# Optimization experiments

Hardware: AMD Instinct MI355X
Metric: run time of the kernel (lower is better)

The kernel has to match this reference:

```python
import jax, jax.numpy as jnp
import numpy as np

B, N, D_MAX_LEN, D_LENGTH, D_MODEL, N_CLASS = 16, 1024, 512, 256, 128, 10
SAMPLE_K = 140  # factor(20) * ceil(ln(1024)) = 20*7; also n_top u (L_Q == L_K)


def setup_inputs() -> dict:
    key = jax.random.key(0)
    ks = jax.random.split(key, 10)
    s = 0.02
    return {
        "input_embedding": jax.random.normal(ks[0], (B, N, D_MAX_LEN), jnp.float32),
        "index_sample": jax.random.randint(ks[1], (N, SAMPLE_K), 0, N),
        # weights stored [in, out] (transpose of torch Linear.weight)
        "W_lin": jax.random.normal(ks[2], (D_MAX_LEN, D_LENGTH), jnp.float32) * s,
        "b_lin": jnp.zeros((D_LENGTH,), jnp.float32),
        "W_q": jax.random.normal(ks[3], (D_LENGTH, D_MODEL), jnp.float32) * s,
        "W_k": jax.random.normal(ks[4], (D_LENGTH, D_MODEL), jnp.float32) * s,
        "W_v": jax.random.normal(ks[5], (D_LENGTH, D_MODEL), jnp.float32) * s,
        "W_add": jax.random.normal(ks[6], (D_LENGTH, D_MODEL), jnp.float32) * s,
        "b_add": jnp.zeros((D_MODEL,), jnp.float32),
        "W_final": jax.random.normal(ks[7], (D_MODEL * N, N_CLASS), jnp.float32) * s,
        "b_final": jnp.zeros((N_CLASS,), jnp.float32),
    }


def reference(input_embedding, index_sample, W_lin, b_lin, W_q, W_k, W_v,
              W_add, b_add, W_final, b_final):
    # self.linear: [B, N, d_max_len] -> [B, N, d_length]
    x = input_embedding @ W_lin + b_lin
    b, n, _ = x.shape
    # single head (h=1): [B, 1, L, D]
    Q = (x @ W_q)[:, None]
    K = (x @ W_k)[:, None]
    V = (x @ W_v)[:, None]
    d = Q.shape[-1]
    L_K = n
    n_top = index_sample.shape[1]  # u == sample_k here

    # _prob_QK: gather sampled keys per query row, score against Q
    Kg = K[:, :, index_sample, :]                      # [B,1,L_Q,S,D]
    QK_sample = jnp.einsum('bhld,bhlsd->bhls', Q, Kg)  # [B,1,L_Q,S]
    M = QK_sample.max(-1) - QK_sample.sum(-1) / L_K    # sparsity measure
    _, M_top = jax.lax.top_k(M, n_top)                 # [B,1,u]

    Qr = jnp.take_along_axis(Q, M_top[..., None], axis=2)       # [B,1,u,D]
    scores = jnp.einsum('bhud,bhkd->bhuk', Qr, K) / np.sqrt(d)  # [B,1,u,L_K]

    # _get_initial_context (mask_flag=False): mean of V broadcast over L_Q
    ctx = jnp.broadcast_to(V.mean(axis=2, keepdims=True), V.shape)  # [B,1,L_Q,D]

    # _update_context: scatter softmax(scores) @ V into selected rows
    attn = jax.nn.softmax(scores, axis=-1)
    upd = jnp.einsum('bhuk,bhkd->bhud', attn, V)  # [B,1,u,D]
    bidx = jnp.arange(b)[:, None, None]
    hidx = jnp.arange(1)[None, :, None]
    ctx = ctx.at[bidx, hidx, M_top].set(upd)

    ctx = ctx[:, 0]                    # H=1 -> [B,N,D]
    out = ctx + (x @ W_add + b_add)    # residual add (dropout: eval mode)
    out = out.reshape(b, -1) @ W_final + b_final  # [B, n_class]
    return out
```

## Files before the change

kernel.cpp:

```cpp
#include <hip/hip_runtime.h>

typedef __attribute__((ext_vector_type(8))) short short8;
typedef __attribute__((ext_vector_type(8))) unsigned short ushort8;
typedef __attribute__((ext_vector_type(4))) float f32x4;
typedef unsigned short u16;
typedef unsigned int u32;
typedef __attribute__((address_space(1))) const u32 gu32;
typedef __attribute__((address_space(3))) u32 lu32;

__device__ __forceinline__ u16 f2bf(float f){
  unsigned u = __float_as_uint(f);
  u += 0x7FFF + ((u >> 16) & 1);
  return (u16)(u >> 16);
}
__device__ __forceinline__ float bf2f(u16 h){ return __uint_as_float(((unsigned)h) << 16); }

#define BB   16
#define NN   1024
#define DML  512
#define DL   256
#define DM   128
#define NC   10
#define SK   140
#define KTOT (NN*DM)

__global__ void k_prep(const float* __restrict__ Wlin, const float* __restrict__ Wq,
                       const float* __restrict__ Wk, const float* __restrict__ Wv,
                       const float* __restrict__ Wadd,
                       u16* __restrict__ wlinT, u16* __restrict__ w4T,
                       const float* __restrict__ Wf, u16* __restrict__ wf2,
                       const int* __restrict__ idxs, u16* __restrict__ idxp){
  int blk = blockIdx.x, t = threadIdx.x;
  if (blk < 512){
    int id = blk*256 + t;
    {
      int j = id >> 9;
      int k = id & 511;
      wlinT[id] = f2bf(Wlin[k*DL + j]);
    }
    {
      int j = id >> 8;
      int k = id & 255;
      const float* src = (j < 128) ? Wq : (j < 256) ? Wk : (j < 384) ? Wv : Wadd;
      int jj = j & 127;
      w4T[id] = f2bf(src[k*DM + jj]);
    }
  } else if (blk < 1792){
    int i4 = (blk-512)*256 + t;
    float4 v = ((const float4*)Wf)[i4];
    ushort4 o; o.x=f2bf(v.x); o.y=f2bf(v.y); o.z=f2bf(v.z); o.w=f2bf(v.w);
    ((ushort4*)wf2)[i4] = o;
  } else {
    int id = (blk-1792)*256 + t;
    int l = id / 144;
    int s = id - l*144;
    idxp[id] = (s < SK) ? (u16)idxs[l*SK + s] : (u16)0xFFFF;
  }
}

__device__ __forceinline__ void stage2(const u16* __restrict__ A, const u16* __restrict__ B,
                                       int K, int m0, int n0, int kb,
                                       u16* sA, u16* sB, int tid, int wave){
  #pragma unroll
  for (int i = 0; i < 4; ++i){
    int ci  = i*256 + tid;
    int row = ci >> 3;
    int kc  = (ci & 7) ^ (row & 7);
    __builtin_amdgcn_global_load_lds((gu32*)(A + (long)(m0+row)*K + kb + kc*8),
                                     (lu32*)(sA + (i*256 + wave*64)*8), 16, 0, 0);
    __builtin_amdgcn_global_load_lds((gu32*)(B + (long)(n0+row)*K + kb + kc*8),
                                     (lu32*)(sB + (i*256 + wave*64)*8), 16, 0, 0);
  }
}
__device__ __forceinline__ void compute64(const u16* sA, const u16* sB,
                                          int lane, int wrow, int wcol, f32x4 acc[4][4]){
  #pragma unroll
  for (int kk = 0; kk < 2; ++kk){
    short8 af[4], bfr[4];
    int cb = kk*4 + (lane >> 4);
    #pragma unroll
    for (int m_=0; m_<4; ++m_){
      int row = wrow + m_*16 + (lane & 15);
      af[m_] = *(const short8*)&sA[row*64 + ((cb ^ (row & 7)) << 3)];
    }
    #pragma unroll
    for (int n_=0; n_<4; ++n_){
      int row = wcol + n_*16 + (lane & 15);
      bfr[n_] = *(const short8*)&sB[row*64 + ((cb ^ (row & 7)) << 3)];
    }
    #pragma unroll
    for (int m_=0; m_<4; ++m_)
      #pragma unroll
      for (int n_=0; n_<4; ++n_)
        acc[m_][n_] = __builtin_amdgcn_mfma_f32_16x16x32_bf16(af[m_], bfr[n_], acc[m_][n_], 0, 0, 0);
  }
}
__device__ __forceinline__ void gemm_core_db(const u16* __restrict__ A, const u16* __restrict__ B,
                                             int K, int m0, int n0,
                                             u16* sA0, u16* sB0, u16* sA1, u16* sB1,
                                             f32x4 acc[4][4]){
  const int tid  = threadIdx.x;
  const int lane = tid & 63;
  const int wave = tid >> 6;
  const int wrow = (wave >> 1) * 64;
  const int wcol = (wave & 1) * 64;
  u16 *cA = sA0, *cB = sB0, *nA = sA1, *nB = sB1;
  stage2(A, B, K, m0, n0, 0, cA, cB, tid, wave);
  __syncthreads();
  int nt = K >> 6;
  for (int t = 0; t < nt-1; ++t){
    stage2(A, B, K, m0, n0, (t+1)*64, nA, nB, tid, wave);
    compute64(cA, cB, lane, wrow, wcol, acc);
    __syncthreads();
    u16* x;
    x = cA; cA = nA; nA = x;
    x = cB; cB = nB; nB = x;
  }
  compute64(cA, cB, lane, wrow, wcol, acc);
}

__global__ __launch_bounds__(256) void k_gemm_x(const float* __restrict__ A, const u16* __restrict__ B,
                                                const float* __restrict__ bias, u16* __restrict__ out){
  __shared__ u16 smem[12288];
  u16* sA = smem;
  u16* sB = smem + 4096;
  const int tid  = threadIdx.x;
  const int lane = tid & 63;
  const int wave = tid >> 6;
  const int wrow = (wave >> 1) * 32;
  const int wcol = (wave & 1) * 64;
  int m0 = blockIdx.x*64, n0 = blockIdx.y*128;
  f32x4 acc[2][4];
  f32x4 z = {0.f,0.f,0.f,0.f};
  #pragma unroll
  for (int m_=0;m_<2;++m_) for (int n_=0;n_<4;++n_) acc[m_][n_] = z;

  f32x4 ra[4];
  short8 rb[4];
  const int arow = tid >> 2, aq = tid & 3;

  {
    const float* src = A + (long)(m0+arow)*DML + aq*16;
    ra[0] = ((const f32x4*)src)[0]; ra[1] = ((const f32x4*)src)[1];
    ra[2] = ((const f32x4*)src)[2]; ra[3] = ((const f32x4*)src)[3];
    #pragma unroll
    for (int i=0;i<4;++i){
      int ci = i*256 + tid, row = ci>>3, kc = ci&7;
      rb[i] = *(const short8*)(B + (long)(n0+row)*DML + kc*8);
    }
  }
  {
    short8 o0, o1;
    #pragma unroll
    for (int j=0;j<4;++j){ o0[j]=(short)f2bf(ra[0][j]); o0[4+j]=(short)f2bf(ra[1][j]);
                           o1[j]=(short)f2bf(ra[2][j]); o1[4+j]=(short)f2bf(ra[3][j]); }
    int kc0 = aq*2, kc1 = aq*2+1;
    *(short8*)&sA[arow*64 + ((kc0 ^ (arow&7))<<3)] = o0;
    *(short8*)&sA[arow*64 + ((kc1 ^ (arow&7))<<3)] = o1;
    #pragma unroll
    for (int i=0;i<4;++i){
      int ci = i*256 + tid, row = ci>>3, kc = ci&7;
      *(short8*)&sB[row*64 + ((kc ^ (row&7))<<3)] = rb[i];
    }
  }
  __syncthreads();

  for (int tt = 0; tt < 8; ++tt){
    if (tt < 7){
      int kb = (tt+1)*64;
      const float* src = A + (long)(m0+arow)*DML + kb + aq*16;
      ra[0] = ((const f32x4*)src)[0]; ra[1] = ((const f32x4*)src)[1];
      ra[2] = ((const f32x4*)src)[2]; ra[3] = ((const f32x4*)src)[3];
      #pragma unroll
      for (int i=0;i<4;++i){
        int ci = i*256 + tid, row = ci>>3, kc = ci&7;
        rb[i] = *(const short8*)(B + (long)(n0+row)*DML + kb + kc*8);
      }
    }
    #pragma unroll
    for (int kk = 0; kk < 2; ++kk){
      short8 af[2], bfr[4];
      int cb = kk*4 + (lane >> 4);
      #pragma unroll
      for (int m_=0; m_<2; ++m_){
        int row = wrow + m_*16 + (lane & 15);
        af[m_] = *(const short8*)&sA[row*64 + ((cb ^ (row & 7)) << 3)];
      }
      #pragma unroll
      for (int n_=0; n_<4; ++n_){
        int row = wcol + n_*16 + (lane & 15);
        bfr[n_] = *(const short8*)&sB[row*64 + ((cb ^ (row & 7)) << 3)];
      }
      #pragma unroll
      for (int m_=0; m_<2; ++m_)
        #pragma unroll
        for (int n_=0; n_<4; ++n_)
          acc[m_][n_] = __builtin_amdgcn_mfma_f32_16x16x32_bf16(af[m_], bfr[n_], acc[m_][n_], 0, 0, 0);
    }
    __syncthreads();
    if (tt < 7){
      short8 o0, o1;
      #pragma unroll
      for (int j=0;j<4;++j){ o0[j]=(short)f2bf(ra[0][j]); o0[4+j]=(short)f2bf(ra[1][j]);
                             o1[j]=(short)f2bf(ra[2][j]); o1[4+j]=(short)f2bf(ra[3][j]); }
      int kc0 = aq*2, kc1 = aq*2+1;
      *(short8*)&sA[arow*64 + ((kc0 ^ (arow&7))<<3)] = o0;
      *(short8*)&sA[arow*64 + ((kc1 ^ (arow&7))<<3)] = o1;
      #pragma unroll
      for (int i=0;i<4;++i){
        int ci = i*256 + tid, row = ci>>3, kc = ci&7;
        *(short8*)&sB[row*64 + ((kc ^ (row&7))<<3)] = rb[i];
      }
      __syncthreads();
    }
  }

  u16* sC = sB;
  #pragma unroll
  for (int m_=0;m_<2;++m_)
    #pragma unroll
    for (int n_=0;n_<4;++n_)
      #pragma unroll
      for (int rr=0;rr<4;++rr){
        int row = wrow + m_*16 + (lane>>4)*4 + rr;
        int col = wcol + n_*16 + (lane & 15);
        sC[row*128 + col] = f2bf(acc[m_][n_][rr] + bias[n0 + col]);
      }
  __syncthreads();
  #pragma unroll
  for (int i = 0; i < 4; ++i){
    int ci = i*256 + tid;
    int row = ci >> 4, c = ci & 15;
    *(short8*)(out + (long)(m0+row)*DL + n0 + c*8) = *(const short8*)&sC[row*128 + c*8];
  }
}

__global__ __launch_bounds__(256) void k_gemm_qkva(const u16* __restrict__ A, const u16* __restrict__ B,
                                                   const float* __restrict__ badd,
                                                   u16* __restrict__ oq, u16* __restrict__ ok,
                                                   u16* __restrict__ ov, u16* __restrict__ oa){
  __shared__ u16 smem[32768];
  f32x4 acc[4][4];
  f32x4 z = {0.f,0.f,0.f,0.f};
  #pragma unroll
  for (int m_=0;m_<4;++m_) for (int n_=0;n_<4;++n_) acc[m_][n_] = z;
  int m0 = blockIdx.x*128;
  int tn = blockIdx.y;
  gemm_core_db(A, B, DL, m0, tn*128, smem, smem+8192, smem+16384, smem+24576, acc);
  int tid = threadIdx.x, lane = tid & 63, wave = tid >> 6;
  int wrow = (wave>>1)*64, wcol = (wave&1)*64;
  u16* dst = (tn==0) ? oq : (tn==1) ? ok : (tn==2) ? ov : oa;

  u16* sC = smem;
  #pragma unroll
  for (int m_=0;m_<4;++m_)
    #pragma unroll
    for (int n_=0;n_<4;++n_)
      #pragma unroll
      for (int r=0;r<4;++r){
        int row = wrow + m_*16 + (lane>>4)*4 + r;
        int col = wcol + n_*16 + (lane & 15);
        float v = acc[m_][n_][r];
        if (tn == 3) v += badd[col];
        sC[row*128 + col] = f2bf(v);
      }
  __syncthreads();
  u16* db = dst + (long)m0*DM;
  #pragma unroll
  for (int i = 0; i < 8; ++i){
    int ci = i*256 + tid;
    int row = ci >> 4, c = ci & 15;
    *(short8*)(db + (long)row*DM + c*8) = *(const short8*)&sC[row*128 + c*8];
  }
}

__global__ __launch_bounds__(256) void k_gemm_s(const u16* __restrict__ Q, const u16* __restrict__ Km,
                                                u16* __restrict__ S, const u16* __restrict__ idxp,
                                                float* __restrict__ pmax, float* __restrict__ psum){
  __shared__ u16 smem[16384];
  u16* sA = smem;
  u16* sB = smem + 8192;
  const int tid = threadIdx.x, lane = tid & 63, wave = tid >> 6;
  const int wrow = (wave>>1)*64, wcol = (wave&1)*64;
  f32x4 acc[4][4];
  f32x4 z = {0.f,0.f,0.f,0.f};
  #pragma unroll
  for (int m_=0;m_<4;++m_) for (int n_=0;n_<4;++n_) acc[m_][n_] = z;
  int b = blockIdx.x, n0 = blockIdx.y*128, m0 = blockIdx.z*128;
  const u16* A = Q  + (long)b*NN*DM;
  const u16* B = Km + (long)b*NN*DM;

  stage2(A, B, DM, m0, n0, 0, sA, sB, tid, wave);
  __syncthreads();
  compute64(sA, sB, lane, wrow, wcol, acc);
  __syncthreads();
  stage2(A, B, DM, m0, n0, 64, sA, sB, tid, wave);
  __syncthreads();
  compute64(sA, sB, lane, wrow, wcol, acc);
  __syncthreads();

  u16* sS = smem;
  #pragma unroll
  for (int m_=0;m_<4;++m_)
    #pragma unroll
    for (int n_=0;n_<4;++n_)
      #pragma unroll
      for (int r=0;r<4;++r){
        int row = wrow + m_*16 + (lane>>4)*4 + r;
        int col = wcol + n_*16 + (lane & 15);
        sS[row*128 + col] = f2bf(acc[m_][n_][r]);
      }
  __syncthreads();

  u16* Sb = S + (long)b*NN*NN + (long)m0*NN + n0;
  #pragma unroll
  for (int i = 0; i < 8; ++i){
    int ci = i*256 + tid;
    int row = ci >> 4, c = ci & 15;
    *(short8*)(Sb + (long)row*NN + c*8) = *(const short8*)&sS[row*128 + c*8];
  }

  int l = tid >> 1, h = tid & 1;
  const u16* ip = idxp + (long)(m0+l)*144 + h*72;
  float mx = -1e30f, sm = 0.f;
  #pragma unroll
  for (int j = 0; j < 9; ++j){
    ushort8 v = *(const ushort8*)(ip + j*8);
    #pragma unroll
    for (int e = 0; e < 8; ++e){
      int d = (int)v[e] - n0;
      if ((unsigned)d < 128u){
        float s = bf2f(sS[l*128 + d]);
        mx = fmaxf(mx, s); sm += s;
      }
    }
  }
  float mo = __shfl_xor(mx, 1), so = __shfl_xor(sm, 1);
  mx = fmaxf(mx, mo); sm += so;
  if (h == 0){
    int o = (b*8 + blockIdx.y)*NN + m0 + l;
    pmax[o] = mx; psum[o] = sm;
  }
}

__global__ __launch_bounds__(256) void k_rankvm(const float* __restrict__ pmax, const float* __restrict__ psum,
                                                int* __restrict__ partial,
                                                const u16* __restrict__ V, float* __restrict__ vmean){
  int blk = blockIdx.x, t = threadIdx.x;
  if (blk < 256){
    __shared__ float Ml[1024];
    int b = blk >> 4, jc = blk & 15;
    #pragma unroll
    for (int r=0;r<4;++r){
      int i = t + r*256;
      float mx = -1e30f, sm = 0.f;
      #pragma unroll
      for (int nb=0;nb<8;++nb){
        mx = fmaxf(mx, pmax[(b*8+nb)*NN + i]);
        sm += psum[(b*8+nb)*NN + i];
      }
      Ml[i] = mx - sm * (1.0f/1024.0f);
    }
    __syncthreads();
    float mi[4];
    int cnt[4] = {0,0,0,0};
    #pragma unroll
    for (int r=0;r<4;++r) mi[r] = Ml[t + r*256];
    int j0 = jc*64;
    for (int j = 0; j < 64; ++j){
      float mj = Ml[j0 + j];
      int jg = j0 + j;
      #pragma unroll
      for (int r=0;r<4;++r){
        int i = t + r*256;
        cnt[r] += (mj > mi[r]) || (mj == mi[r] && jg < i);
      }
    }
    int* pb = partial + (b*16 + jc)*NN;
    #pragma unroll
    for (int r=0;r<4;++r) pb[t + r*256] = cnt[r];
  } else {
    __shared__ float red[16][128];
    int b = blk - 256;
    int d8 = t & 15, seg = t >> 4;
    const u16* Vb = V + (long)b*KTOT + seg*64*DM + d8*8;
    float acc[8] = {0,0,0,0,0,0,0,0};
    for (int l = 0; l < 64; ++l){
      short8 v = *(const short8*)(Vb + l*DM);
      #pragma unroll
      for (int j=0;j<8;++j) acc[j] += bf2f((u16)v[j]);
    }
    #pragma unroll
    for (int j=0;j<8;++j) red[seg][d8*8+j] = acc[j];
    __syncthreads();
    if (t < 128){
      float s = 0.f;
      #pragma unroll
      for (int g=0;g<16;++g) s += red[g][t];
      vmean[b*DM + t] = s * (1.0f/1024.0f);
    }
  }
}

__global__ __launch_bounds__(1024) void k_sel(const int* __restrict__ partial, int* __restrict__ mtop,
                                              int* __restrict__ selmap){
  int b = blockIdx.x, i = threadIdx.x;
  int cnt = 0;
  #pragma unroll
  for (int jc = 0; jc < 16; ++jc) cnt += partial[(b*16 + jc)*NN + i];
  selmap[b*NN + i] = (cnt < SK) ? cnt : -1;
  if (cnt < SK) mtop[b*SK + cnt] = i;
}

__global__ __launch_bounds__(256) void k_attn(const u16* __restrict__ S, const u16* __restrict__ V,
                                              const int* __restrict__ mtop, float* __restrict__ upd){
  __shared__ float sE[4][1024];
  __shared__ float redM[4][4];
  __shared__ float redS[4][4];
  __shared__ float sP[4][4][128];
  int b = blockIdx.x, u0 = blockIdx.y*4, t = threadIdx.x;
  int lane = t & 63, wave = t >> 6;
  const float inv = 0.08838834764831845f;

  int rows[4];
  #pragma unroll
  for (int r=0;r<4;++r) rows[r] = mtop[b*SK + u0 + r];

  float sv[4][4];
  float pm[4];
  const u16* Sb = S + (long)b*NN*NN;
  #pragma unroll
  for (int r=0;r<4;++r){
    ushort4 raw = ((const ushort4*)(Sb + (long)rows[r]*NN))[t];
    sv[r][0] = bf2f(raw.x)*inv; sv[r][1] = bf2f(raw.y)*inv;
    sv[r][2] = bf2f(raw.z)*inv; sv[r][3] = bf2f(raw.w)*inv;
    pm[r] = fmaxf(fmaxf(sv[r][0],sv[r][1]), fmaxf(sv[r][2],sv[r][3]));
  }
  #pragma unroll
  for (int o=32;o;o>>=1)
    #pragma unroll
    for (int r=0;r<4;++r) pm[r] = fmaxf(pm[r], __shfl_xor(pm[r],o));
  if (lane == 0){
    #pragma unroll
    for (int r=0;r<4;++r) redM[wave][r] = pm[r];
  }
  __syncthreads();
  float mx[4], ps[4];
  #pragma unroll
  for (int r=0;r<4;++r)
    mx[r] = fmaxf(fmaxf(redM[0][r],redM[1][r]), fmaxf(redM[2][r],redM[3][r]));
  #pragma unroll
  for (int r=0;r<4;++r){
    float s = 0.f;
    #pragma unroll
    for (int j=0;j<4;++j){
      float e = __expf(sv[r][j] - mx[r]);
      sE[r][t*4+j] = e;
      s += e;
    }
    ps[r] = s;
  }
  #pragma unroll
  for (int o=32;o;o>>=1)
    #pragma unroll
    for (int r=0;r<4;++r) ps[r] += __shfl_xor(ps[r],o);
  if (lane == 0){
    #pragma unroll
    for (int r=0;r<4;++r) redS[wave][r] = ps[r];
  }
  __syncthreads();
  float rZ[4];
  #pragma unroll
  for (int r=0;r<4;++r)
    rZ[r] = 1.0f / (redS[0][r]+redS[1][r]+redS[2][r]+redS[3][r]);

  int dg = t & 15;
  int kg = t >> 4;
  const u16* Vb = V + (long)b*KTOT + dg*8;
  float acc[4][8];
  #pragma unroll
  for (int r=0;r<4;++r)
    #pragma unroll
    for (int j=0;j<8;++j) acc[r][j] = 0.f;

  for (int k = kg; k < NN; k += 16){
    short8 v = *(const short8*)(Vb + (long)k*DM);
    float vf[8];
    #pragma unroll
    for (int j=0;j<8;++j) vf[j] = bf2f((u16)v[j]);
    #pragma unroll
    for (int r=0;r<4;++r){
      float e = sE[r][k];
      #pragma unroll
      for (int j=0;j<8;++j) acc[r][j] += e * vf[j];
    }
  }

  #pragma unroll
  for (int o=16;o<64;o<<=1)
    #pragma unroll
    for (int r=0;r<4;++r)
      #pragma unroll
      for (int j=0;j<8;++j) acc[r][j] += __shfl_xor(acc[r][j], o);

  if ((t & 63) < 16){
    #pragma unroll
    for (int r=0;r<4;++r)
      #pragma unroll
      for (int j=0;j<8;++j) sP[wave][r][dg*8+j] = acc[r][j];
  }
  __syncthreads();
  if (t < 128){
    #pragma unroll
    for (int r=0;r<4;++r){
      float s = sP[0][r][t] + sP[1][r][t] + sP[2][r][t] + sP[3][r][t];
      upd[((long)b*SK + u0 + r)*DM + t] = s * rZ[r];
    }
  }
}

__global__ __launch_bounds__(256) void k_final(const float* __restrict__ upd, const float* __restrict__ vmean,
                                               const int* __restrict__ selmap,
                                               const u16* __restrict__ Aad,
                                               const u16* __restrict__ wf2, float* __restrict__ part){
  int b = blockIdx.x, ch = blockIdx.y, t = threadIdx.x;
  long base = (long)b * KTOT;
  int k0 = ch * 4096;
  float acc[NC] = {0.f};
  for (int k = k0 + t; k < k0 + 4096; k += 256){
    int l = k >> 7, d = k & 127;
    int sel = selmap[b*NN + l];
    float c = (sel >= 0) ? upd[((long)b*SK + sel)*DM + d] : vmean[b*DM + d];
    float v = c + bf2f(Aad[base + k]);
    const u32* w32 = (const u32*)(wf2 + (long)k*NC);
    #pragma unroll
    for (int cc = 0; cc < 5; ++cc){
      u32 w = w32[cc];
      acc[2*cc]   += v * bf2f((u16)(w & 0xFFFF));
      acc[2*cc+1] += v * bf2f((u16)(w >> 16));
    }
  }
  __shared__ float lred[40];
  int lane = t & 63, wave = t >> 6;
  #pragma unroll
  for (int c = 0; c < NC; ++c){
    float v = acc[c];
    #pragma unroll
    for (int o=32;o;o>>=1) v += __shfl_xor(v,o);
    if (lane == 0) lred[wave*NC + c] = v;
  }
  __syncthreads();
  if (t < NC) part[(b*32 + ch)*NC + t] = lred[t] + lred[NC+t] + lred[2*NC+t] + lred[3*NC+t];
}

__global__ void k_out(const float* __restrict__ part, const float* __restrict__ bfin, float* __restrict__ out){
  int t = threadIdx.x;
  if (t < BB*NC){
    int b = t / NC, c = t % NC;
    float s = bfin[c];
    #pragma unroll
    for (int ch = 0; ch < 32; ++ch) s += part[(b*32 + ch)*NC + c];
    out[t] = s;
  }
}

extern "C" void kernel_launch(void* const* d_in, const int* in_sizes, int n_in,
                              void* d_out, int out_size, void* d_ws, size_t ws_size,
                              hipStream_t stream){
  const float* emb  = (const float*)d_in[0];
  const int*   idxs = (const int*)  d_in[1];
  const float* Wlin = (const float*)d_in[2];
  const float* blin = (const float*)d_in[3];
  const float* Wq   = (const float*)d_in[4];
  const float* Wk   = (const float*)d_in[5];
  const float* Wv   = (const float*)d_in[6];
  const float* Wadd = (const float*)d_in[7];
  const float* badd = (const float*)d_in[8];
  const float* Wfin = (const float*)d_in[9];
  const float* bfin = (const float*)d_in[10];
  float* out = (float*)d_out;

  char* p = (char*)d_ws;
  auto alloc = [&](size_t bytes)->char*{ char* r = p; p += (bytes + 255) & ~(size_t)255; return r; };
  u16*   wlinT  = (u16*)  alloc((size_t)DL*DML*2);
  u16*   w4T    = (u16*)  alloc((size_t)4*DM*DL*2);
  u16*   x_bf   = (u16*)  alloc((size_t)BB*NN*DL*2);
  u16*   q_bf   = (u16*)  alloc((size_t)BB*NN*DM*2);
  u16*   k_bf   = (u16*)  alloc((size_t)BB*NN*DM*2);
  u16*   v_bf   = (u16*)  alloc((size_t)BB*NN*DM*2);
  u16*   a_bf   = (u16*)  alloc((size_t)BB*NN*DM*2);
  u16*   s_bf   = (u16*)  alloc((size_t)BB*NN*NN*2);
  u16*   idxp   = (u16*)  alloc((size_t)NN*144*2);
  float* pmax   = (float*)alloc((size_t)BB*8*NN*4);
  float* psum   = (float*)alloc((size_t)BB*8*NN*4);
  int*   rankp  = (int*)  alloc((size_t)BB*16*NN*4);
  int*   mtop   = (int*)  alloc((size_t)BB*SK*4);
  int*   selmap = (int*)  alloc((size_t)BB*NN*4);
  float* vmean  = (float*)alloc((size_t)BB*DM*4);
  float* upd    = (float*)alloc((size_t)BB*SK*DM*4);
  u16*   wf2    = (u16*)  alloc((size_t)KTOT*NC*2);
  float* part   = (float*)alloc((size_t)BB*32*NC*4);

  k_prep<<<dim3(2368), dim3(256), 0, stream>>>(Wlin, Wq, Wk, Wv, Wadd, wlinT, w4T, Wfin, wf2, idxs, idxp);
  k_gemm_x<<<dim3(256, 2), dim3(256), 0, stream>>>(emb, wlinT, blin, x_bf);
  k_gemm_qkva<<<dim3(128, 4), dim3(256), 0, stream>>>(x_bf, w4T, badd, q_bf, k_bf, v_bf, a_bf);
  k_gemm_s<<<dim3(16, 8, 8), dim3(256), 0, stream>>>(q_bf, k_bf, s_bf, idxp, pmax, psum);
  k_rankvm<<<dim3(272), dim3(256), 0, stream>>>(pmax, psum, rankp, v_bf, vmean);
  k_sel<<<dim3(BB), dim3(1024), 0, stream>>>(rankp, mtop, selmap);
  k_attn<<<dim3(BB, SK/4), dim3(256), 0, stream>>>(s_bf, v_bf, mtop, upd);
  k_final<<<dim3(BB, 32), dim3(256), 0, stream>>>(upd, vmean, selmap, a_bf, wf2, part);
  k_out<<<dim3(1), dim3(256), 0, stream>>>(part, bfin, out);
}
```

Baseline: 104.8 us.

## Compute top-u attention with bf16 MFMA over transposed V tiles

The QKVA GEMM epilogue now also writes a transposed copy of V (d-major) through a padded shared-memory tile. The attention kernel handles 16 selected query rows per block instead of 4 and computes exp(scores)·V with 16x16x32 bf16 MFMA. V tiles are streamed into LDS via global_load_lds with an XOR swizzle, and the exponentiated probabilities are staged as bf16. This replaces scalar FMA loops that reread V for every 4 rows, cutting V traffic and ALU work. The cost is an extra transposed-V write and bf16 rounding of the softmax weights before the product.

```diff
diff --git a/kernel.cpp b/kernel.cpp
--- a/kernel.cpp
+++ b/kernel.cpp
@@ -238,7 +238,8 @@
 __global__ __launch_bounds__(256) void k_gemm_qkva(const u16* __restrict__ A, const u16* __restrict__ B,
                                                    const float* __restrict__ badd,
                                                    u16* __restrict__ oq, u16* __restrict__ ok,
-                                                   u16* __restrict__ ov, u16* __restrict__ oa){
+                                                   u16* __restrict__ ov, u16* __restrict__ oa,
+                                                   u16* __restrict__ vT){
   __shared__ u16 smem[32768];
   f32x4 acc[4][4];
   f32x4 z = {0.f,0.f,0.f,0.f};
@@ -251,6 +252,7 @@
   int wrow = (wave>>1)*64, wcol = (wave&1)*64;
   u16* dst = (tn==0) ? oq : (tn==1) ? ok : (tn==2) ? ov : oa;
 
+  __syncthreads();
   u16* sC = smem;
   #pragma unroll
   for (int m_=0;m_<4;++m_)
@@ -262,7 +264,7 @@
         int col = wcol + n_*16 + (lane & 15);
         float v = acc[m_][n_][r];
         if (tn == 3) v += badd[col];
-        sC[row*128 + col] = f2bf(v);
+        sC[row*136 + col] = f2bf(v);
       }
   __syncthreads();
   u16* db = dst + (long)m0*DM;
@@ -270,7 +272,20 @@
   for (int i = 0; i < 8; ++i){
     int ci = i*256 + tid;
     int row = ci >> 4, c = ci & 15;
-    *(short8*)(db + (long)row*DM + c*8) = *(const short8*)&sC[row*128 + c*8];
+    *(short8*)(db + (long)row*DM + c*8) = *(const short8*)&sC[row*136 + c*8];
+  }
+  if (tn == 2){
+    int b2 = m0 >> 10, l0 = m0 & 1023;
+    u16* vtb = vT + (long)b2*KTOT + l0;
+    #pragma unroll
+    for (int i = 0; i < 8; ++i){
+      int gi = i*256 + tid;
+      int d = gi >> 4, mc = gi & 15;
+      ushort8 o;
+      #pragma unroll
+      for (int j = 0; j < 8; ++j) o[j] = sC[(mc*8+j)*136 + d];
+      *(ushort8*)(vtb + (long)d*NN + mc*8) = o;
+    }
   }
 }
 
@@ -412,109 +427,95 @@
   if (cnt < SK) mtop[b*SK + cnt] = i;
 }
 
-__global__ __launch_bounds__(256) void k_attn(const u16* __restrict__ S, const u16* __restrict__ V,
+__global__ __launch_bounds__(256) void k_attn(const u16* __restrict__ S, const u16* __restrict__ vT,
                                               const int* __restrict__ mtop, float* __restrict__ upd){
-  __shared__ float sE[4][1024];
-  __shared__ float redM[4][4];
-  __shared__ float redS[4][4];
-  __shared__ float sP[4][4][128];
-  int b = blockIdx.x, u0 = blockIdx.y*4, t = threadIdx.x;
+  __shared__ u16 sPt[2][16*72];
+  __shared__ u16 sVt[128*64];
+  __shared__ int   sBrow[16];
+  __shared__ float sMx[16];
+  __shared__ float sSum[16];
+  int b = blockIdx.x, u0 = blockIdx.y*16, t = threadIdx.x;
   int lane = t & 63, wave = t >> 6;
   const float inv = 0.08838834764831845f;
 
-  int rows[4];
-  #pragma unroll
-  for (int r=0;r<4;++r) rows[r] = mtop[b*SK + u0 + r];
-
-  float sv[4][4];
-  float pm[4];
-  const u16* Sb = S + (long)b*NN*NN;
-  #pragma unroll
-  for (int r=0;r<4;++r){
-    ushort4 raw = ((const ushort4*)(Sb + (long)rows[r]*NN))[t];
-    sv[r][0] = bf2f(raw.x)*inv; sv[r][1] = bf2f(raw.y)*inv;
-    sv[r][2] = bf2f(raw.z)*inv; sv[r][3] = bf2f(raw.w)*inv;
-    pm[r] = fmaxf(fmaxf(sv[r][0],sv[r][1]), fmaxf(sv[r][2],sv[r][3]));
-  }
-  #pragma unroll
-  for (int o=32;o;o>>=1)
-    #pragma unroll
-    for (int r=0;r<4;++r) pm[r] = fmaxf(pm[r], __shfl_xor(pm[r],o));
-  if (lane == 0){
-    #pragma unroll
-    for (int r=0;r<4;++r) redM[wave][r] = pm[r];
-  }
-  __syncthreads();
-  float mx[4], ps[4];
-  #pragma unroll
-  for (int r=0;r<4;++r)
-    mx[r] = fmaxf(fmaxf(redM[0][r],redM[1][r]), fmaxf(redM[2][r],redM[3][r]));
-  #pragma unroll
-  for (int r=0;r<4;++r){
-    float s = 0.f;
-    #pragma unroll
-    for (int j=0;j<4;++j){
-      float e = __expf(sv[r][j] - mx[r]);
-      sE[r][t*4+j] = e;
-      s += e;
-    }
-    ps[r] = s;
-  }
-  #pragma unroll
-  for (int o=32;o;o>>=1)
-    #pragma unroll
-    for (int r=0;r<4;++r) ps[r] += __shfl_xor(ps[r],o);
-  if (lane == 0){
-    #pragma unroll
-    for (int r=0;r<4;++r) redS[wave][r] = ps[r];
-  }
-  __syncthreads();
-  float rZ[4];
-  #pragma unroll
-  for (int r=0;r<4;++r)
-    rZ[r] = 1.0f / (redS[0][r]+redS[1][r]+redS[2][r]+redS[3][r]);
-
-  int dg = t & 15;
-  int kg = t >> 4;
-  const u16* Vb = V + (long)b*KTOT + dg*8;
-  float acc[4][8];
-  #pragma unroll
-  for (int r=0;r<4;++r)
-    #pragma unroll
-    for (int j=0;j<8;++j) acc[r][j] = 0.f;
-
-  for (int k = kg; k < NN; k += 16){
-    short8 v = *(const short8*)(Vb + (long)k*DM);
-    float vf[8];
-    #pragma unroll
-    for (int j=0;j<8;++j) vf[j] = bf2f((u16)v[j]);
-    #pragma unroll
-    for (int r=0;r<4;++r){
-      float e = sE[r][k];
-      #pragma unroll
-      for (int j=0;j<8;++j) acc[r][j] += e * vf[j];
-    }
-  }
-
-  #pragma unroll
-  for (int o=16;o<64;o<<=1)
-    #pragma unroll
-    for (int r=0;r<4;++r)
-      #pragma unroll
-      for (int j=0;j<8;++j) acc[r][j] += __shfl_xor(acc[r][j], o);
-
-  if ((t & 63) < 16){
-    #pragma unroll
-    for (int r=0;r<4;++r)
-      #pragma unroll
-      for (int j=0;j<8;++j) sP[wave][r][dg*8+j] = acc[r][j];
-  }
-  __syncthreads();
-  if (t < 128){
-    #pragma unroll
-    for (int r=0;r<4;++r){
-      float s = sP[0][r][t] + sP[1][r][t] + sP[2][r][t] + sP[3][r][t];
-      upd[((long)b*SK + u0 + r)*DM + t] = s * rZ[r];
+  if (t < 16){
+    int u = u0 + t; if (u > SK-1) u = SK-1;
+    sBrow[t] = mtop[b*SK + u];
+  }
+  __syncthreads();
+  int row = t >> 4, c = t & 15;
+  const u16* Srow = S + (long)b*NN*NN + (long)sBrow[row]*NN;
+
+  float mx = -1e30f;
+  #pragma unroll
+  for (int j = 0; j < 8; ++j){
+    ushort8 v = *(const ushort8*)(Srow + c*8 + j*128);
+    #pragma unroll
+    for (int e = 0; e < 8; ++e) mx = fmaxf(mx, bf2f((u16)v[e]));
+  }
+  #pragma unroll
+  for (int o = 1; o < 16; o <<= 1) mx = fmaxf(mx, __shfl_xor(mx, o));
+  if (c == 0) sMx[row] = mx;
+  __syncthreads();
+  float mxr = sMx[row] * inv;
+  const u16* vTb = vT + (long)b*KTOT;
+
+  f32x4 acc[2];
+  f32x4 z = {0.f,0.f,0.f,0.f};
+  acc[0] = z; acc[1] = z;
+  float ps = 0.f;
+
+  for (int ks = 0; ks < 16; ++ks){
+    #pragma unroll
+    for (int i = 0; i < 4; ++i){
+      int ci = i*256 + t;
+      int r2 = ci >> 3;
+      int kc = (ci & 7) ^ (r2 & 7);
+      __builtin_amdgcn_global_load_lds((gu32*)(vTb + (long)r2*NN + ks*64 + kc*8),
+                                       (lu32*)(sVt + (i*256 + wave*64)*8), 16, 0, 0);
+    }
+    u16* sp = sPt[ks & 1];
+    {
+      ushort4 s4 = *(const ushort4*)(Srow + ks*64 + c*4);
+      float e0 = __expf(bf2f(s4.x)*inv - mxr);
+      float e1 = __expf(bf2f(s4.y)*inv - mxr);
+      float e2 = __expf(bf2f(s4.z)*inv - mxr);
+      float e3 = __expf(bf2f(s4.w)*inv - mxr);
+      ps += e0+e1+e2+e3;
+      ushort4 pw; pw.x=f2bf(e0); pw.y=f2bf(e1); pw.z=f2bf(e2); pw.w=f2bf(e3);
+      *(ushort4*)&sp[row*72 + c*4] = pw;
+    }
+    __syncthreads();
+    #pragma unroll
+    for (int kk = 0; kk < 2; ++kk){
+      int cb = kk*4 + (lane >> 4);
+      short8 af = *(const short8*)&sp[(lane & 15)*72 + cb*8];
+      #pragma unroll
+      for (int n_ = 0; n_ < 2; ++n_){
+        int r2 = wave*32 + n_*16 + (lane & 15);
+        short8 bf_ = *(const short8*)&sVt[r2*64 + ((cb ^ (r2 & 7)) << 3)];
+        acc[n_] = __builtin_amdgcn_mfma_f32_16x16x32_bf16(af, bf_, acc[n_], 0, 0, 0);
+      }
+    }
+    __syncthreads();
+  }
+
+  #pragma unroll
+  for (int o = 1; o < 16; o <<= 1) ps += __shfl_xor(ps, o);
+  if (c == 0) sSum[row] = ps;
+  __syncthreads();
+  int r0 = (lane >> 4) * 4;
+  float rz[4];
+  #pragma unroll
+  for (int r = 0; r < 4; ++r) rz[r] = 1.0f / sSum[r0 + r];
+  #pragma unroll
+  for (int n_ = 0; n_ < 2; ++n_){
+    int col = wave*32 + n_*16 + (lane & 15);
+    #pragma unroll
+    for (int r = 0; r < 4; ++r){
+      int urow = u0 + r0 + r;
+      if (urow < SK)
+        upd[((long)b*SK + urow)*DM + col] = acc[n_][r] * rz[r];
     }
   }
 }
@@ -589,6 +590,7 @@
   u16*   k_bf   = (u16*)  alloc((size_t)BB*NN*DM*2);
   u16*   v_bf   = (u16*)  alloc((size_t)BB*NN*DM*2);
   u16*   a_bf   = (u16*)  alloc((size_t)BB*NN*DM*2);
+  u16*   vT     = (u16*)  alloc((size_t)BB*KTOT*2);
   u16*   s_bf   = (u16*)  alloc((size_t)BB*NN*NN*2);
   u16*   idxp   = (u16*)  alloc((size_t)NN*144*2);
   float* pmax   = (float*)alloc((size_t)BB*8*NN*4);
@@ -603,11 +605,11 @@
 
   k_prep<<<dim3(2368), dim3(256), 0, stream>>>(Wlin, Wq, Wk, Wv, Wadd, wlinT, w4T, Wfin, wf2, idxs, idxp);
   k_gemm_x<<<dim3(256, 2), dim3(256), 0, stream>>>(emb, wlinT, blin, x_bf);
-  k_gemm_qkva<<<dim3(128, 4), dim3(256), 0, stream>>>(x_bf, w4T, badd, q_bf, k_bf, v_bf, a_bf);
+  k_gemm_qkva<<<dim3(128, 4), dim3(256), 0, stream>>>(x_bf, w4T, badd, q_bf, k_bf, v_bf, a_bf, vT);
   k_gemm_s<<<dim3(16, 8, 8), dim3(256), 0, stream>>>(q_bf, k_bf, s_bf, idxp, pmax, psum);
   k_rankvm<<<dim3(272), dim3(256), 0, stream>>>(pmax, psum, rankp, v_bf, vmean);
   k_sel<<<dim3(BB), dim3(1024), 0, stream>>>(rankp, mtop, selmap);
-  k_attn<<<dim3(BB, SK/4), dim3(256), 0, stream>>>(s_bf, v_bf, mtop, upd);
+  k_attn<<<dim3(BB, 9), dim3(256), 0, stream>>>(s_bf, vT, mtop, upd);
   k_final<<<dim3(BB, 32), dim3(256), 0, stream>>>(upd, vmean, selmap, a_bf, wf2, part);
   k_out<<<dim3(1), dim3(256), 0, stream>>>(part, bfin, out);
 }
```

New measurement: 97.58 us. -6.9%, faster.
